# Performance work log

Measured on AMD Instinct MI355X. Metric: run time of the kernel, lower is better.

The kernel has to match this reference:

```python
import jax, jax.numpy as jnp
import numpy as np

B, L, H, N, CH = 8, 2048, 512, 64, 1


def setup_inputs() -> dict:
    key = jax.random.key(0)
    ks = jax.random.split(key, 7)
    # S4D-Lin style init: w = -0.5 + i*pi*n, with slight noise on the real part
    w_re = -(0.5 + 0.1 * jax.random.uniform(ks[0], (H, N), dtype=jnp.float32))
    w_im = jnp.broadcast_to(jnp.pi * jnp.arange(N, dtype=jnp.float32), (H, N)).copy()
    C_re = jax.random.normal(ks[1], (CH, H, N), dtype=jnp.float32)
    C_im = jax.random.normal(ks[2], (CH, H, N), dtype=jnp.float32)
    D = jax.random.normal(ks[3], (CH, H), dtype=jnp.float32)
    # log-uniform dt in [1e-3, 1e-1]
    log_dt = jax.random.uniform(ks[4], (H,), dtype=jnp.float32,
                                minval=jnp.log(1e-3), maxval=jnp.log(1e-1))
    dt = jnp.exp(log_dt)
    u = jax.random.normal(ks[5], (B, L, H), dtype=jnp.float32)
    return {"u": u, "w_re": w_re, "w_im": w_im, "C_re": C_re,
            "C_im": C_im, "D": D, "dt": dt}


def reference(u, w_re, w_im, C_re, C_im, D, dt):
    # u: [B, L, H] -> [B, H, L]
    uT = jnp.swapaxes(u, -1, -2)
    l = uT.shape[-1]
    h = dt.shape[-1]
    w = (w_re + 1j * w_im).astype(jnp.complex64)          # [t, n]
    v = h // w.shape[0]
    w = jnp.tile(w, (v, 1))                                # [h, n]
    C = (C_re + 1j * C_im).astype(jnp.complex64)           # [c, h, n]
    # --- kernel generation ---
    dtA = w * dt[:, None]                                  # [h, n]
    K = jnp.arange(l) * dtA[..., None]                     # [h, n, l]
    Cs = C * ((jnp.exp(dtA) - 1.0) / w)                    # [c, h, n]
    k = 2.0 * jnp.einsum('chn,hnl->chl', Cs, jnp.exp(K)).real  # [c, h, l]
    # --- FFT convolution ---
    k_f = jnp.fft.rfft(k, n=2 * l - 1)                     # [c, h, l]
    u_f = jnp.fft.rfft(uT, n=2 * l - 1)                    # [B, h, l]
    y_f = jnp.einsum('...hl,chl->...chl', u_f, k_f)        # [B, c, h, l]
    y = jnp.fft.irfft(y_f, n=2 * l)[..., :l]               # [B, c, h, l]
    # skip connection
    y = y + jnp.einsum('...hl,ch->...chl', uT, D)
    # '... c h l -> ... l c h'
    return jnp.moveaxis(y, (-3, -2, -1), (-2, -1, -3))
```

## Files before the change

### kernel.cpp

```cpp
#include <hip/hip_runtime.h>
#include <hip/hip_bf16.h>
#include <math.h>


namespace {
constexpr int cB = 8;
constexpr int cL = 2048;
constexpr int cH = 512;
constexpr int cN = 64;
constexpr int M1 = 4095;
constexpr int M2 = 4096;
constexpr int BH = cB * cH;
constexpr int MA = BH + cH;

constexpr size_t S0   = 2 * ((size_t)cH * cN * 6);
constexpr size_t S_B1 = S0;
constexpr size_t S_A  = S_B1 + (size_t)4096 * 2048;
constexpr size_t S_T2 = S_A  + (size_t)MA * 2048;
constexpr size_t S_U  = S_T2 + (size_t)2048 * 4096;
}

typedef __attribute__((ext_vector_type(8))) short short8;
typedef __attribute__((ext_vector_type(2))) short sh2;
typedef __attribute__((ext_vector_type(4))) float f32x4;

static __device__ inline short f2bf(float x) {
    __hip_bfloat16 h = __float2bfloat16(x);
    return *reinterpret_cast<short*>(&h);
}
static __device__ inline float bf2f(short s) {
    return __uint_as_float(((unsigned int)(unsigned short)s) << 16);
}
static __device__ __forceinline__ void load_lds16(const short* g, short* l) {
    __builtin_amdgcn_global_load_lds(
        (const __attribute__((address_space(1))) void*)g,
        (__attribute__((address_space(3))) void*)l, 16, 0, 0);
}
#define WAIT_LGKM0() do { asm volatile("s_waitcnt lgkmcnt(0)" ::: "memory"); \
                          __builtin_amdgcn_sched_barrier(0); } while (0)
#define WAIT_VM(n)   do { asm volatile("s_waitcnt vmcnt(" #n ")" ::: "memory"); \
                          __builtin_amdgcn_sched_barrier(0); } while (0)
#define BAR() __builtin_amdgcn_s_barrier()

__global__ __launch_bounds__(256) void k_tabs(short* __restrict__ Wb)
{
    int tid = threadIdx.x;
    if (blockIdx.x < 2048) {
        int j  = blockIdx.x;
        int base = (j < 1024) ? 4 * j : (j == 1024 ? 2 : 4 * (2048 - j) + 2);
        int t0 = tid * 8;
        int p0 = (int)(((long)j * t0) % M1);
        float c, s, cs, ss;
        sincosf((6.283185307179586f / (float)M1) * (float)p0, &s, &c);
        sincosf((6.283185307179586f / (float)M1) * (float)j,  &ss, &cs);
        short8 vc, vs;
#pragma unroll
        for (int i = 0; i < 8; ++i) {
            vc[i] = f2bf(c); vs[i] = f2bf(s);
            float tr = c * cs - s * ss;
            s = c * ss + s * cs;
            c = tr;
        }
        *(short8*)&Wb[S_B1 + (size_t)base       * 2048 + t0] = vc;
        *(short8*)&Wb[S_B1 + (size_t)(base + 1) * 2048 + t0] = vs;
    } else {
        int r   = blockIdx.x - 2048;
        int p   = r >> 10, tau = r & 1023;
        int t   = 2 * tau + p;
        int k0  = tid * 8;
        float stepang = (6.283185307179586f / (float)M2) * (float)t;
        float cs, ss; sincosf(stepang, &ss, &cs);
        short8 v;
        if (k0 < 1024) {
            int ph = (k0 * t) & (M2 - 1);
            float c, s; sincosf((6.283185307179586f / (float)M2) * (float)ph, &s, &c);
#pragma unroll
            for (int i = 0; i < 8; ++i) {
                v[i] = f2bf(c);
                float tr = c * cs - s * ss;
                s = c * ss + s * cs;
                c = tr;
            }
        } else {
            int j0 = k0 - 1024;
            int ph = (j0 * t) & (M2 - 1);
            float c, s; sincosf((6.283185307179586f / (float)M2) * (float)ph, &s, &c);
#pragma unroll
            for (int i = 0; i < 8; ++i) {
                int k = k0 + i;
                v[i] = (k == 1024) ? f2bf((tau & 1) ? -1.f : 1.f) : f2bf(s);
                float tr = c * cs - s * ss;
                s = c * ss + s * cs;
                c = tr;
            }
        }
        *(short8*)&Wb[S_T2 + (size_t)r * 2048 + k0] = v;
    }
}

__global__ __launch_bounds__(256) void k_trans(const float* __restrict__ u,
                                               short* __restrict__ Wb)
{
    __shared__ float tile[64][65];
    int t0 = blockIdx.x * 64;
    int h0 = blockIdx.y * 64;
    int b  = blockIdx.z;
    int cx = threadIdx.x & 63, r0 = threadIdx.x >> 6;
#pragma unroll
    for (int i = 0; i < 16; ++i) {
        int row = r0 + i * 4;
        tile[row][cx] = u[((size_t)b * cL + t0 + row) * cH + h0 + cx];
    }
    __syncthreads();
    short* A = Wb + S_A;
#pragma unroll
    for (int i = 0; i < 16; ++i) {
        int hrow = r0 + i * 4;
        A[(size_t)(b * cH + h0 + hrow) * 2048 + t0 + cx] = f2bf(tile[cx][hrow]);
    }
}

__global__ __launch_bounds__(256) void k_kgen(
    const float* __restrict__ w_re, const float* __restrict__ w_im,
    const float* __restrict__ C_re, const float* __restrict__ C_im,
    const float* __restrict__ dt, short* __restrict__ Wb)
{
    __shared__ float md[cN * 6];
    int h = blockIdx.x, tid = threadIdx.x;
    if (tid < cN) {
        int idx = h * cN + tid;
        double dtv = dt[h];
        double wr = w_re[idx], wi = w_im[idx];
        double ar = wr * dtv, ai = wi * dtv;
        double er = exp(ar);
        double zs, zc; sincos(ai, &zs, &zc);
        double zr = er * zc, zi = er * zs;
        double nr = zr - 1.0, ni = zi;
        double inv = 1.0 / (wr * wr + wi * wi);
        double gr = (nr * wr + ni * wi) * inv;
        double gi = (ni * wr - nr * wi) * inv;
        double cr = C_re[idx], ci = C_im[idx];
        md[tid*6+0] = (float)(cr * gr - ci * gi);
        md[tid*6+1] = (float)(cr * gi + ci * gr);
        md[tid*6+2] = (float)zr; md[tid*6+3] = (float)zi;
        md[tid*6+4] = (float)ar; md[tid*6+5] = (float)ai;
    }
    __syncthreads();
    int t0 = tid * 8;
    float acc[8] = {0.f, 0.f, 0.f, 0.f, 0.f, 0.f, 0.f, 0.f};
    for (int n = 0; n < cN; ++n) {
        float csr = md[n*6+0], csi = md[n*6+1];
        float zr  = md[n*6+2], zi  = md[n*6+3];
        float ar  = md[n*6+4], ai  = md[n*6+5];
        float mag = expf(ar * (float)t0);
        double ph = fmod((double)ai * (double)t0, 6.283185307179586);
        float s, c; sincosf((float)ph, &s, &c);
        float pr = mag * c, pi = mag * s;
#pragma unroll
        for (int i = 0; i < 8; ++i) {
            acc[i] += csr * pr - csi * pi;
            float tr = pr * zr - pi * zi;
            pi = pr * zi + pi * zr;
            pr = tr;
        }
    }
    short8 v;
#pragma unroll
    for (int i = 0; i < 8; ++i) v[i] = f2bf(2.f * acc[i]);
    *reinterpret_cast<short8*>(&Wb[S_A + (size_t)(BH + h) * 2048 + t0]) = v;
}

#define MFMA16(AR, BR, ACC) \
    _Pragma("unroll") for (int kk = 0; kk < 2; ++kk) \
    _Pragma("unroll") for (int ni = 0; ni < 2; ++ni) \
    _Pragma("unroll") for (int mi = 0; mi < 4; ++mi) \
        ACC[mi][ni] = __builtin_amdgcn_mfma_f32_16x16x32_bf16(AR[mi][kk], BR[ni][kk], ACC[mi][ni], 0, 0, 0);

__device__ __forceinline__ void gemm8p_core(
    const short* __restrict__ Ag, int lda,
    const short* __restrict__ Bg, int ldb,
    int m0, int n0, int nt, short* lds, f32x4 (&acc)[4][4][2])
{
    const int tid  = threadIdx.x;
    const int wave = tid >> 6, lane = tid & 63;
    const int wm = wave >> 2, wn = wave & 3;
    const int lm = lane & 15, lk = lane >> 4;
    const int srow8 = lane >> 3;
    const int scol  = (lane & 7) * 8;

    auto stage = [&](const short* G, int ldg, int row0, int half, int kt, int sb) {
        short* l0 = lds + sb + (size_t)((kt & 1) * 2 + half) * 8192;
#pragma unroll
        for (int q = 0; q < 2; ++q) {
            int chunk = wave * 2 + q;
            int r = chunk * 8 + srow8;
            int c = scol ^ ((r & 7) << 3);
            load_lds16(G + (size_t)(row0 + half * 128 + r) * ldg + kt * 64 + c,
                       l0 + chunk * 512);
        }
    };
    auto rdA = [&](int qa, int kt, int mi, int kk) -> short8 {
        int rl = wm * 64 + mi * 16 + lm;
        int c  = (kk * 32 + lk * 8) ^ ((rl & 7) << 3);
        return *(const short8*)(lds + (size_t)((kt & 1) * 2 + qa) * 8192 + rl * 64 + c);
    };
    auto rdB = [&](int qb, int kt, int ni, int kk) -> short8 {
        int rl = wn * 32 + ni * 16 + lm;
        int c  = (kk * 32 + lk * 8) ^ ((rl & 7) << 3);
        return *(const short8*)(lds + 32768 + (size_t)((kt & 1) * 2 + qb) * 8192 + rl * 64 + c);
    };

    stage(Ag, lda, m0, 0, 0, 0);
    stage(Bg, ldb, n0, 0, 0, 32768);
    stage(Bg, ldb, n0, 1, 0, 32768);
    stage(Ag, lda, m0, 1, 0, 0);
    stage(Ag, lda, m0, 0, 1, 0);
    stage(Bg, ldb, n0, 0, 1, 32768);
    stage(Bg, ldb, n0, 1, 1, 32768);
    stage(Ag, lda, m0, 1, 1, 0);
    WAIT_VM(12);
    BAR();

    short8 a0[4][2], a1[4][2], b0[2][2], b1[2][2];
    for (int t = 0; t < nt; ++t) {
        const bool st = (t + 2 < nt);
#pragma unroll
        for (int mi = 0; mi < 4; ++mi) { a0[mi][0] = rdA(0, t, mi, 0); a0[mi][1] = rdA(0, t, mi, 1); }
#pragma unroll
        for (int ni = 0; ni < 2; ++ni) { b0[ni][0] = rdB(0, t, ni, 0); b0[ni][1] = rdB(0, t, ni, 1); }
        BAR();
        WAIT_LGKM0();
        __builtin_amdgcn_s_setprio(1);
        MFMA16(a0, b0, acc[0]);
        __builtin_amdgcn_s_setprio(0);
        if (st) { WAIT_VM(10); } else { WAIT_VM(0); }
        BAR();
#pragma unroll
        for (int ni = 0; ni < 2; ++ni) { b1[ni][0] = rdB(1, t, ni, 0); b1[ni][1] = rdB(1, t, ni, 1); }
        if (st) { stage(Ag, lda, m0, 0, t + 2, 0); stage(Bg, ldb, n0, 0, t + 2, 32768); }
        BAR();
        WAIT_LGKM0();
        __builtin_amdgcn_s_setprio(1);
        MFMA16(a0, b1, acc[1]);
        __builtin_amdgcn_s_setprio(0);
        if (st) { WAIT_VM(12); } else { WAIT_VM(0); }
        BAR();
#pragma unroll
        for (int mi = 0; mi < 4; ++mi) { a1[mi][0] = rdA(1, t, mi, 0); a1[mi][1] = rdA(1, t, mi, 1); }
        if (st) stage(Bg, ldb, n0, 1, t + 2, 32768);
        BAR();
        WAIT_LGKM0();
        __builtin_amdgcn_s_setprio(1);
        MFMA16(a1, b1, acc[3]);
        __builtin_amdgcn_s_setprio(0);
        BAR();
        if (st) stage(Ag, lda, m0, 1, t + 2, 0);
        __builtin_amdgcn_s_setprio(1);
        MFMA16(a1, b0, acc[2]);
        __builtin_amdgcn_s_setprio(0);
        if (st) { WAIT_VM(12); } else { WAIT_VM(0); }
        BAR();
    }
}

__global__ __launch_bounds__(512, 2) void k_fwd8(short* __restrict__ Wb)
{
    __shared__ short lds_s[65536];
    int tile = (blockIdx.x & 7) * 32 + (blockIdx.x >> 3);
    const int m0 = (tile >> 4) * 256, n0 = (tile & 15) * 256;
    const int tid = threadIdx.x;
    const int wave = tid >> 6, lane = tid & 63;
    const int wm = wave >> 2, wn = wave & 3;
    const int lm = lane & 15, lk = lane >> 4;

    f32x4 acc[4][4][2] = {};
    gemm8p_core(Wb + S_A, 2048, Wb + S_B1, 2048, m0, n0, 32, lds_s, acc);

    short* Uw = Wb + S_U;
    const short* KF = Wb + S_U;
    short (*M)[136] = (short(*)[136])lds_s;
    for (int q = 0; q < 4; ++q) {
        __syncthreads();
#pragma unroll
        for (int mi = 0; mi < 4; ++mi)
#pragma unroll
        for (int ni = 0; ni < 2; ++ni)
#pragma unroll
        for (int r = 0; r < 4; ++r)
            M[wm * 64 + mi * 16 + lk * 4 + r][wn * 32 + ni * 16 + lm] =
                f2bf(acc[q][mi][ni][r]);
        __syncthreads();
        const int pq0 = (n0 >> 2) + (q & 1) * 32;
#pragma unroll
        for (int pass = 0; pass < 4; ++pass) {
            int rl = pass * 32 + (tid >> 4);
            int cp = (tid & 15) * 2;
            int rowg = m0 + (q >> 1) * 128 + rl;
            int h = rowg & (cH - 1);
            int colg = n0 + (q & 1) * 128 + cp * 4;
            short8 kf8 = *(const short8*)&KF[(size_t)(4096 + h) * 4096 + colg];
            short8 m8  = *(const short8*)&M[rl][cp * 4];
            sh2 vce, vco, vse, vso;
#pragma unroll
            for (int i = 0; i < 2; ++i) {
                float C  = bf2f(m8[4*i]),   S  = bf2f(m8[4*i+1]);
                float C2 = bf2f(m8[4*i+2]), S2 = bf2f(m8[4*i+3]);
                float Ck  = bf2f(kf8[4*i]),   Sk  = bf2f(kf8[4*i+1]);
                float Ck2 = bf2f(kf8[4*i+2]), Sk2 = bf2f(kf8[4*i+3]);
                int p = pq0 + cp + i;
                float scp = (p == 0 ? 1.0f : 2.0f) * (1.0f / (float)M2);
                float scq = 2.0f / (float)M2;
                float yrp = scp * (Ck * C - Sk * S);
                float yip = scp * (Ck * S + Sk * C);
                float yrq = scq * (Ck2 * C2 - Sk2 * S2);
                float yiq = scq * (Ck2 * S2 + Sk2 * C2);
                float ce, co, se, so;
                if (p == 0) { ce = yrp; co = yrp; se = yrq; so = yiq; }
                else { ce = yrp + yrq; co = yrp - yrq; se = yip - yiq; so = yip + yiq; }
                vce[i] = f2bf(ce); vco[i] = f2bf(co);
                vse[i] = f2bf(se); vso[i] = f2bf(so);
            }
            size_t base = (size_t)rowg * 4096;
            int kx = pq0 + cp;
            *(sh2*)&Uw[base + kx]        = vce;
            *(sh2*)&Uw[base + 1024 + kx] = vse;
            *(sh2*)&Uw[base + 2048 + kx] = vco;
            *(sh2*)&Uw[base + 3072 + kx] = vso;
        }
    }
}

__global__ __launch_bounds__(256, 2) void k_kfg(short* __restrict__ Wb)
{
    __shared__ __align__(16) short As[128][32];
    __shared__ __align__(16) short Bs[128][32];
    const short* A = Wb + S_A;
    const short* B = Wb + S_B1;
    short* U = Wb + S_U;
    const int tid = threadIdx.x;
    const int m0 = 4096 + blockIdx.y * 128, n0 = blockIdx.x * 128;
    const int wave = tid >> 6, lane = tid & 63;
    const int wr = wave >> 1, wc = wave & 1;
    const int lm = lane & 15, lk = lane >> 4;
    const int srow = lane >> 2, scol = (lane & 3) * 8;

    f32x4 acc[4][4] = {};
    for (int k0 = 0; k0 < 2048; k0 += 32) {
        __syncthreads();
        {
            int c0 = wave * 2;
            load_lds16(&A[(size_t)(m0 + c0*16      + srow)*2048 + k0 + scol], &As[c0*16][0]);
            load_lds16(&A[(size_t)(m0 + c0*16 + 16 + srow)*2048 + k0 + scol], &As[c0*16+16][0]);
            load_lds16(&B[(size_t)(n0 + c0*16      + srow)*2048 + k0 + scol], &Bs[c0*16][0]);
            load_lds16(&B[(size_t)(n0 + c0*16 + 16 + srow)*2048 + k0 + scol], &Bs[c0*16+16][0]);
        }
        __syncthreads();
        short8 a[4];
#pragma unroll
        for (int mi = 0; mi < 4; ++mi)
            a[mi] = *(const short8*)&As[wr*64 + mi*16 + lm][lk*8];
#pragma unroll
        for (int ni = 0; ni < 4; ++ni) {
            short8 b = *(const short8*)&Bs[wc*64 + ni*16 + lm][lk*8];
#pragma unroll
            for (int mi = 0; mi < 4; ++mi)
                acc[mi][ni] = __builtin_amdgcn_mfma_f32_16x16x32_bf16(a[mi], b, acc[mi][ni], 0, 0, 0);
        }
    }
#pragma unroll
    for (int mi = 0; mi < 4; ++mi)
#pragma unroll
    for (int ni = 0; ni < 4; ++ni)
#pragma unroll
    for (int r = 0; r < 4; ++r) {
        int row = m0 + wr*64 + mi*16 + lk*4 + r;
        int col = n0 + wc*64 + ni*16 + lm;
        U[(size_t)row * 4096 + col] = f2bf(acc[mi][ni][r]);
    }
}

__global__ __launch_bounds__(512, 1) void k_invB(const float* __restrict__ u,
                                                 const float* __restrict__ Dp,
                                                 short* __restrict__ Wb,
                                                 float* __restrict__ out)
{
    __shared__ short lds_s[57344];
    int tile = (blockIdx.x & 7) * 32 + (blockIdx.x >> 3);
    const int m0   = (tile >> 4) * 256;
    const int rest = tile & 15;
    const int p    = rest >> 3;
    const int n0   = (rest & 7) * 128;
    const int tid = threadIdx.x;
    const int wave = tid >> 6, lane = tid & 63;
    const int wm = wave >> 2, wn = wave & 3;
    const int lm = lane & 15, lk = lane >> 4;
    const int srow8 = lane >> 3;
    const int scol  = (lane & 7) * 8;
    constexpr int nt = 32;
    short* lds = lds_s;
    const short* Ag = Wb + S_U + (size_t)p * 2048;
    const short* Bg = Wb + S_T2 + (size_t)p * 1024 * 2048;

    auto stageA = [&](int half, int kt) {
        short* l0 = lds + (size_t)((kt & 1) * 2 + half) * 8192;
#pragma unroll
        for (int q = 0; q < 2; ++q) {
            int chunk = wave * 2 + q;
            int r = chunk * 8 + srow8;
            int c = scol ^ ((r & 7) << 3);
            load_lds16(Ag + (size_t)(m0 + half * 128 + r) * 4096 + kt * 64 + c,
                       l0 + chunk * 512);
        }
    };
    auto stageB = [&](int kt, int slot) {
        short* l0 = lds + 32768 + (size_t)slot * 8192;
#pragma unroll
        for (int q = 0; q < 2; ++q) {
            int chunk = wave * 2 + q;
            int r = chunk * 8 + srow8;
            int c = scol ^ ((r & 7) << 3);
            load_lds16(Bg + (size_t)(n0 + r) * 2048 + kt * 64 + c,
                       l0 + chunk * 512);
        }
    };
    auto rdA = [&](int half, int kt, int mi, int kk) -> short8 {
        int rl = wm * 64 + mi * 16 + lm;
        int c  = (kk * 32 + lk * 8) ^ ((rl & 7) << 3);
        return *(const short8*)(lds + (size_t)((kt & 1) * 2 + half) * 8192 + rl * 64 + c);
    };
    auto rdB = [&](int slot, int ni, int kk) -> short8 {
        int rl = wn * 32 + ni * 16 + lm;
        int c  = (kk * 32 + lk * 8) ^ ((rl & 7) << 3);
        return *(const short8*)(lds + 32768 + (size_t)slot * 8192 + rl * 64 + c);
    };

    f32x4 acc[2][4][2] = {};

    stageA(0, 0);
    stageB(0, 0);
    stageA(1, 0);
    stageA(0, 1);
    stageB(1, 1);
    stageB(2, 2);
    WAIT_VM(6);
    BAR();

    short8 a[4][2], b[2][2];
    int bs = 0;
    for (int t = 0; t < nt; ++t) {
        const bool deep = (t + 3 < nt);
#pragma unroll
        for (int mi = 0; mi < 4; ++mi) { a[mi][0] = rdA(0, t, mi, 0); a[mi][1] = rdA(0, t, mi, 1); }
#pragma unroll
        for (int ni = 0; ni < 2; ++ni) { b[ni][0] = rdB(bs, ni, 0); b[ni][1] = rdB(bs, ni, 1); }
        if (t + 1 < nt) stageA(1, t + 1);
        BAR();
        WAIT_LGKM0();
        __builtin_amdgcn_s_setprio(1);
        MFMA16(a, b, acc[0]);
        __builtin_amdgcn_s_setprio(0);
        if (deep) { WAIT_VM(6); } else { WAIT_VM(0); }
        BAR();
#pragma unroll
        for (int mi = 0; mi < 4; ++mi) { a[mi][0] = rdA(1, t, mi, 0); a[mi][1] = rdA(1, t, mi, 1); }
        if (t + 2 < nt) stageA(0, t + 2);
        if (t + 3 < nt) stageB(t + 3, bs);
        BAR();
        WAIT_LGKM0();
        __builtin_amdgcn_s_setprio(1);
        MFMA16(a, b, acc[1]);
        __builtin_amdgcn_s_setprio(0);
        if (deep) { WAIT_VM(6); } else { WAIT_VM(0); }
        BAR();
        bs = (bs == 2) ? 0 : bs + 1;
    }

    const int b_  = m0 >> 9;
    const int h00 = m0 & 511;
    float (*T)[132] = (float(*)[132])lds_s;
#pragma unroll
    for (int q = 0; q < 2; ++q) {
        __syncthreads();
#pragma unroll
        for (int mi = 0; mi < 4; ++mi)
#pragma unroll
        for (int ni = 0; ni < 2; ++ni) {
            int tl = wn * 32 + ni * 16 + lm;
            int hl = wm * 64 + mi * 16 + lk * 4;
            *(float4*)&T[tl][hl] = *(float4*)&acc[q][mi][ni];
        }
        __syncthreads();
        int hg = h00 + q * 128 + (tid & 31) * 4;
        float4 dv = *(const float4*)&Dp[hg];
#pragma unroll
        for (int it = 0; it < 8; ++it) {
            int tl = (tid >> 5) + it * 16;
            int tg = 2 * (n0 + tl) + p;
            size_t gidx = ((size_t)b_ * cL + tg) * cH + hg;
            float4 uv = *(const float4*)&u[gidx];
            float4 yv = *(float4*)&T[tl][(tid & 31) * 4];
            yv.x += dv.x * uv.x;
            yv.y += dv.y * uv.y;
            yv.z += dv.z * uv.z;
            yv.w += dv.w * uv.w;
            *(float4*)&out[gidx] = yv;
        }
    }
}

extern "C" void kernel_launch(void* const* d_in, const int* in_sizes, int n_in,
                              void* d_out, int out_size, void* d_ws, size_t ws_size,
                              hipStream_t stream) {
    const float* u    = (const float*)d_in[0];
    const float* w_re = (const float*)d_in[1];
    const float* w_im = (const float*)d_in[2];
    const float* C_re = (const float*)d_in[3];
    const float* C_im = (const float*)d_in[4];
    const float* Dp   = (const float*)d_in[5];
    const float* dt   = (const float*)d_in[6];
    float* out = (float*)d_out;
    short* Wb  = (short*)d_ws;

    hipLaunchKernelGGL(k_tabs,  dim3(4096), dim3(256), 0, stream, Wb);
    hipLaunchKernelGGL(k_trans, dim3(cL / 64, cH / 64, cB), dim3(256), 0, stream, u, Wb);
    hipLaunchKernelGGL(k_kgen,  dim3(cH), dim3(256), 0, stream,
                       w_re, w_im, C_re, C_im, dt, Wb);
    hipLaunchKernelGGL(k_kfg,   dim3(32, 4), dim3(256), 0, stream, Wb);
    hipLaunchKernelGGL(k_fwd8,  dim3(256), dim3(512), 0, stream, Wb);
    hipLaunchKernelGGL(k_invB,  dim3(256), dim3(512), 0, stream, u, Dp, Wb, out);
}
```

Baseline: 202.9 us.

## Software-pipeline LDS fragment reads one step ahead of MFMA in both GEMM cores

Restructures the main loops of both GEMM cores so LDS fragment reads for the next sub-step or next k-tile are issued before the current MFMA block. Partial lgkmcnt waits replace full drains, and the vmcnt waits and barriers are reshuffled to match. The aim is to hide LDS read latency behind matrix math. It costs extra register buffers (next-B copies, separate A buffers), which may raise register pressure, and the hand-tuned wait counts risk races if miscounted.

```diff
diff --git a/kernel.cpp b/kernel.cpp
--- a/kernel.cpp
+++ b/kernel.cpp
@@ -37,6 +37,8 @@
         (__attribute__((address_space(3))) void*)l, 16, 0, 0);
 }
 #define WAIT_LGKM0() do { asm volatile("s_waitcnt lgkmcnt(0)" ::: "memory"); \
+                          __builtin_amdgcn_sched_barrier(0); } while (0)
+#define WAIT_LGKM(n) do { asm volatile("s_waitcnt lgkmcnt(" #n ")" ::: "memory"); \
                           __builtin_amdgcn_sched_barrier(0); } while (0)
 #define WAIT_VM(n)   do { asm volatile("s_waitcnt vmcnt(" #n ")" ::: "memory"); \
                           __builtin_amdgcn_sched_barrier(0); } while (0)
@@ -221,44 +223,59 @@
     WAIT_VM(12);
     BAR();
 
-    short8 a0[4][2], a1[4][2], b0[2][2], b1[2][2];
+    short8 a0[4][2], a1[4][2], b0[2][2], b1[2][2], b0n[2][2];
+#pragma unroll
+    for (int mi = 0; mi < 4; ++mi) { a0[mi][0] = rdA(0, 0, mi, 0); a0[mi][1] = rdA(0, 0, mi, 1); }
+#pragma unroll
+    for (int ni = 0; ni < 2; ++ni) { b0[ni][0] = rdB(0, 0, ni, 0); b0[ni][1] = rdB(0, 0, ni, 1); }
+    WAIT_VM(10);
+    BAR();
+
     for (int t = 0; t < nt; ++t) {
         const bool st = (t + 2 < nt);
-#pragma unroll
-        for (int mi = 0; mi < 4; ++mi) { a0[mi][0] = rdA(0, t, mi, 0); a0[mi][1] = rdA(0, t, mi, 1); }
-#pragma unroll
-        for (int ni = 0; ni < 2; ++ni) { b0[ni][0] = rdB(0, t, ni, 0); b0[ni][1] = rdB(0, t, ni, 1); }
-        BAR();
-        WAIT_LGKM0();
+        const bool rd = (t + 1 < nt);
+#pragma unroll
+        for (int ni = 0; ni < 2; ++ni) { b1[ni][0] = rdB(1, t, ni, 0); b1[ni][1] = rdB(1, t, ni, 1); }
+        BAR();
+        WAIT_LGKM(4);
         __builtin_amdgcn_s_setprio(1);
         MFMA16(a0, b0, acc[0]);
         __builtin_amdgcn_s_setprio(0);
-        if (st) { WAIT_VM(10); } else { WAIT_VM(0); }
-        BAR();
-#pragma unroll
-        for (int ni = 0; ni < 2; ++ni) { b1[ni][0] = rdB(1, t, ni, 0); b1[ni][1] = rdB(1, t, ni, 1); }
+        if (rd) { WAIT_VM(8); } else { WAIT_VM(0); }
+        BAR();
+#pragma unroll
+        for (int mi = 0; mi < 4; ++mi) { a1[mi][0] = rdA(1, t, mi, 0); a1[mi][1] = rdA(1, t, mi, 1); }
         if (st) { stage(Ag, lda, m0, 0, t + 2, 0); stage(Bg, ldb, n0, 0, t + 2, 32768); }
         BAR();
-        WAIT_LGKM0();
+        WAIT_LGKM(8);
         __builtin_amdgcn_s_setprio(1);
         MFMA16(a0, b1, acc[1]);
         __builtin_amdgcn_s_setprio(0);
-        if (st) { WAIT_VM(12); } else { WAIT_VM(0); }
-        BAR();
-#pragma unroll
-        for (int mi = 0; mi < 4; ++mi) { a1[mi][0] = rdA(1, t, mi, 0); a1[mi][1] = rdA(1, t, mi, 1); }
+        BAR();
         if (st) stage(Bg, ldb, n0, 1, t + 2, 32768);
         BAR();
         WAIT_LGKM0();
         __builtin_amdgcn_s_setprio(1);
         MFMA16(a1, b1, acc[3]);
         __builtin_amdgcn_s_setprio(0);
-        BAR();
+        if (st) { WAIT_VM(10); } else { WAIT_VM(0); }
+        BAR();
+        if (rd) {
+#pragma unroll
+            for (int mi = 0; mi < 4; ++mi) { a0[mi][0] = rdA(0, t + 1, mi, 0); a0[mi][1] = rdA(0, t + 1, mi, 1); }
+#pragma unroll
+            for (int ni = 0; ni < 2; ++ni) { b0n[ni][0] = rdB(0, t + 1, ni, 0); b0n[ni][1] = rdB(0, t + 1, ni, 1); }
+        }
         if (st) stage(Ag, lda, m0, 1, t + 2, 0);
+        BAR();
         __builtin_amdgcn_s_setprio(1);
         MFMA16(a1, b0, acc[2]);
         __builtin_amdgcn_s_setprio(0);
-        if (st) { WAIT_VM(12); } else { WAIT_VM(0); }
+        if (rd) {
+#pragma unroll
+            for (int ni = 0; ni < 2; ++ni) { b0[ni][0] = b0n[ni][0]; b0[ni][1] = b0n[ni][1]; }
+            WAIT_VM(10);
+        } else { WAIT_VM(0); }
         BAR();
     }
 }
@@ -442,37 +459,53 @@
     stageA(0, 1);
     stageB(1, 1);
     stageB(2, 2);
-    WAIT_VM(6);
+    WAIT_VM(8);
     BAR();
-
-    short8 a[4][2], b[2][2];
+    short8 a0[4][2], a1[4][2], b[2][2], bn[2][2];
+#pragma unroll
+    for (int mi = 0; mi < 4; ++mi) { a0[mi][0] = rdA(0, 0, mi, 0); a0[mi][1] = rdA(0, 0, mi, 1); }
+#pragma unroll
+    for (int ni = 0; ni < 2; ++ni) { b[ni][0] = rdB(0, ni, 0); b[ni][1] = rdB(0, ni, 1); }
+    WAIT_VM(4);
+    BAR();
+
     int bs = 0;
     for (int t = 0; t < nt; ++t) {
-        const bool deep = (t + 3 < nt);
-#pragma unroll
-        for (int mi = 0; mi < 4; ++mi) { a[mi][0] = rdA(0, t, mi, 0); a[mi][1] = rdA(0, t, mi, 1); }
-#pragma unroll
-        for (int ni = 0; ni < 2; ++ni) { b[ni][0] = rdB(bs, ni, 0); b[ni][1] = rdB(bs, ni, 1); }
-        if (t + 1 < nt) stageA(1, t + 1);
-        BAR();
-        WAIT_LGKM0();
+        const bool r1 = (t + 1 < nt);
+        const bool s2 = (t + 2 < nt);
+        const bool s3 = (t + 3 < nt);
+        const bool tail = (t >= nt - 3);
+        const int bs2 = (bs == 2) ? 0 : bs + 1;
+#pragma unroll
+        for (int mi = 0; mi < 4; ++mi) { a1[mi][0] = rdA(1, t, mi, 0); a1[mi][1] = rdA(1, t, mi, 1); }
+        if (r1) stageA(1, t + 1);
+        BAR();
+        WAIT_LGKM(8);
         __builtin_amdgcn_s_setprio(1);
-        MFMA16(a, b, acc[0]);
+        MFMA16(a0, b, acc[0]);
         __builtin_amdgcn_s_setprio(0);
-        if (deep) { WAIT_VM(6); } else { WAIT_VM(0); }
-        BAR();
-#pragma unroll
-        for (int mi = 0; mi < 4; ++mi) { a[mi][0] = rdA(1, t, mi, 0); a[mi][1] = rdA(1, t, mi, 1); }
-        if (t + 2 < nt) stageA(0, t + 2);
-        if (t + 3 < nt) stageB(t + 3, bs);
-        BAR();
-        WAIT_LGKM0();
+        if (tail) { WAIT_VM(0); } else { WAIT_VM(4); }
+        BAR();
+        if (r1) {
+#pragma unroll
+            for (int mi = 0; mi < 4; ++mi) { a0[mi][0] = rdA(0, t + 1, mi, 0); a0[mi][1] = rdA(0, t + 1, mi, 1); }
+#pragma unroll
+            for (int ni = 0; ni < 2; ++ni) { bn[ni][0] = rdB(bs2, ni, 0); bn[ni][1] = rdB(bs2, ni, 1); }
+        }
+        if (s2) stageA(0, t + 2);
+        if (s3) stageB(t + 3, bs);
+        BAR();
+        if (r1) { WAIT_LGKM(12); } else { WAIT_LGKM0(); }
         __builtin_amdgcn_s_setprio(1);
-        MFMA16(a, b, acc[1]);
+        MFMA16(a1, b, acc[1]);
         __builtin_amdgcn_s_setprio(0);
-        if (deep) { WAIT_VM(6); } else { WAIT_VM(0); }
-        BAR();
-        bs = (bs == 2) ? 0 : bs + 1;
+        if (r1) {
+#pragma unroll
+            for (int ni = 0; ni < 2; ++ni) { b[ni][0] = bn[ni][0]; b[ni][1] = bn[ni][1]; }
+        }
+        if (tail) { WAIT_VM(0); } else { WAIT_VM(4); }
+        BAR();
+        bs = bs2;
     }
 
     const int b_  = m0 >> 9;
```

Result: no change. 199.2 us (-1.8%).
